# Performance work log

Hardware: AMD Instinct MI355X
Metric: run time of the kernel (lower is better)

## Reference

```python
import jax, jax.numpy as jnp
import numpy as np

N_NODES = 1000
N_EDGES = 8000
IN_FEATS = 64
HID = 128
RDIM = HID // 2  # UniversalReadout output dim
EPS = 1e-5


def _lrelu(v):
    return jax.nn.leaky_relu(v, 0.01)


def setup_inputs() -> dict:
    key = jax.random.key(0)
    ks = jax.random.split(key, 16)
    B = 128
    node_feats = jax.random.normal(ks[0], (B * N_NODES, IN_FEATS), jnp.float32)
    edge_weights = jax.random.uniform(ks[1], (B * N_EDGES,), jnp.float32)
    g_weights = jax.random.uniform(ks[2], (B * N_NODES,), jnp.float32)
    src = jax.random.randint(ks[3], (N_EDGES,), 0, N_NODES)
    dst = jax.random.randint(ks[4], (N_EDGES,), 0, N_NODES)
    # GraphConv weights (in, out), kaiming-ish scale
    W1 = jax.random.normal(ks[5], (IN_FEATS, HID), jnp.float32) / np.sqrt(IN_FEATS)
    W2 = jax.random.normal(ks[6], (HID, HID), jnp.float32) / np.sqrt(HID)
    W3 = jax.random.normal(ks[7], (HID, HID), jnp.float32) / np.sqrt(HID)
    suppl = jnp.ones((3, N_EDGES), jnp.float32)           # suppl_weights_conv1..3
    AR = jnp.ones((4, N_NODES), jnp.float32)              # AR1..AR4 weights
    gn_gamma = jnp.ones((3, HID), jnp.float32)
    gn_beta = jnp.zeros((3, HID), jnp.float32)
    gn_alpha = jnp.ones((3, HID), jnp.float32)            # GraphNorm mean-scale
    phi_W = jax.random.normal(ks[8], (3, HID, HID), jnp.float32) / np.sqrt(HID)
    phi_b = jnp.zeros((3, HID), jnp.float32)
    rho_W = jax.random.normal(ks[9], (3, HID, RDIM), jnp.float32) / np.sqrt(HID)
    rho_b = jnp.zeros((3, RDIM), jnp.float32)
    return dict(node_feats=node_feats, edge_weights=edge_weights, g_weights=g_weights,
                W1=W1, W2=W2, W3=W3, suppl=suppl, AR=AR,
                gn_gamma=gn_gamma, gn_beta=gn_beta, gn_alpha=gn_alpha,
                phi_W=phi_W, phi_b=phi_b, rho_W=rho_W, rho_b=rho_b,
                src=src, dst=dst)


def _forward(node_feats, edge_weights, g_weights, W1, W2, W3, suppl, AR,
             gn_gamma, gn_beta, gn_alpha, phi_W, phi_b, rho_W, rho_b, src, dst):
    B = node_feats.shape[0] // N_NODES
    x = node_feats.reshape(B, N_NODES, -1)        # (B, N, F)
    gw = g_weights.reshape(B, N_NODES)            # (B, N)
    ew = edge_weights.reshape(B, N_EDGES)         # (B, E)

    # structural degree normalization (norm='both'), shared topology
    deg_out = jnp.maximum(jnp.zeros((N_NODES,), x.dtype).at[src].add(1.0), 1.0)
    deg_in = jnp.maximum(jnp.zeros((N_NODES,), x.dtype).at[dst].add(1.0), 1.0)
    n_out = deg_out ** -0.5
    n_in = deg_in ** -0.5

    def gconv(h, W, ew_l):
        hs = h * n_out[None, :, None]
        msgs = hs[:, src, :] * ew_l[:, :, None]                       # (B, E, D)
        agg = jnp.zeros_like(hs).at[:, dst].add(msgs)                  # scatter-add
        return (agg * n_in[None, :, None]) @ W

    def gnorm(h, i):
        mean = h.mean(axis=1, keepdims=True)
        sub = h - gn_alpha[i] * mean
        var = (sub * sub).mean(axis=1, keepdims=True)
        return gn_gamma[i] * sub * jax.lax.rsqrt(var + EPS) + gn_beta[i]

    def uro(h, i):  # UniversalReadout (deep-sets): per-node MLP -> sum -> MLP
        z = _lrelu(h @ phi_W[i] + phi_b[i]).sum(axis=1)
        return _lrelu(z @ rho_W[i] + rho_b[i])

    def wmean(h, ar):  # dgl.mean_nodes with node weight: mean over nodes of w*x
        w = gw * ar[None, :]
        return (w[:, :, None] * h).mean(axis=1)

    pieces = [wmean(x, AR[0])]
    h = x
    Ws = (W1, W2, W3)
    for i in range(3):
        h = _lrelu(gnorm(gconv(h, Ws[i], ew * suppl[i][None, :]), i))
        pieces.append(uro(h, i))
        pieces.append(wmean(h, AR[i + 1]))
    return _lrelu(jnp.concatenate(pieces, axis=-1))


def reference(node_feats, edge_weights, g_weights, W1, W2, W3, suppl, AR,
              gn_gamma, gn_beta, gn_alpha, phi_W, phi_b, rho_W, rho_b, src, dst):
    return _forward(node_feats, edge_weights, g_weights, W1, W2, W3, suppl, AR,
                    gn_gamma, gn_beta, gn_alpha, phi_W, phi_b, rho_W, rho_b, src, dst)
```

## Files before the change

kernel.cpp:

```cpp
#include <hip/hip_runtime.h>
#include <cstddef>

#define NN 1000
#define NE 8000
#define FIN 64
#define DH 128
#define RD 64
#define FEPS 1e-5f

typedef short short8 __attribute__((ext_vector_type(8)));
typedef float f32x4 __attribute__((ext_vector_type(4)));

__device__ __forceinline__ float lrelu(float x){ return x > 0.f ? x : 0.01f*x; }

__device__ __forceinline__ unsigned short f2b(float x){
  union { float f; unsigned int u; } v; v.f = x;
  unsigned int r = (v.u + 0x7fffu + ((v.u >> 16) & 1u)) >> 16;
  return (unsigned short)r;
}
__device__ __forceinline__ float b2f(unsigned int lo16){
  union { unsigned int u; float f; } v; v.u = lo16 << 16; return v.f;
}
__device__ __forceinline__ unsigned int pack2(float a, float b){
  return (unsigned int)f2b(a) | ((unsigned int)f2b(b) << 16);
}


__global__ __launch_bounds__(1024) void k_topo(const int* __restrict__ src,
                       const int* __restrict__ dst,
                       float* nout, float* nin, int* rp,
                       int* csr_s, int* csr_e, int* csr_d){
  __shared__ int sdo[1024], sdi[1024], ssc[1024], sfill[1024];
  int t = threadIdx.x;
  sdo[t] = 0; sdi[t] = 0;
  __syncthreads();
  for (int e = t; e < NE; e += 1024){
    atomicAdd(&sdo[src[e]], 1);
    atomicAdd(&sdi[dst[e]], 1);
  }
  __syncthreads();
  int d = sdi[t];
  ssc[t] = d; __syncthreads();
  for (int off = 1; off < 1024; off <<= 1){
    int v = (t >= off) ? ssc[t-off] : 0;
    __syncthreads();
    ssc[t] += v;
    __syncthreads();
  }
  int myrp = ssc[t] - d;
  if (t < NN){
    rp[t] = myrp;
    nin[t]  = rsqrtf((float)max(sdi[t], 1));
    nout[t] = rsqrtf((float)max(sdo[t], 1));
  }
  if (t == NN-1) rp[NN] = ssc[t];
  sfill[t] = myrp;
  __syncthreads();
  for (int e = t; e < NE; e += 1024){
    int dn = dst[e];
    int pos = atomicAdd(&sfill[dn], 1);
    csr_s[pos] = src[e];
    csr_e[pos] = e;
    csr_d[pos] = dn;
  }
}


__global__ __launch_bounds__(256) void k_edge(const float* __restrict__ ew,
        const float* __restrict__ sup, const float* __restrict__ nout,
        const float* __restrict__ nin, const int* __restrict__ csr_s,
        const int* __restrict__ csr_e, const int* __restrict__ csr_d,
        int2* __restrict__ ecl, int B){
  int bid = blockIdx.x, t = threadIdx.x;
  int layer, b, q;
  if ((B & 7) == 0){
    int xcd = bid & 7, r = bid >> 3;
    int bsub = r/12, rem = r - bsub*12;
    layer = rem >> 2; q = rem & 3; b = bsub*8 + xcd;
  } else {
    layer = bid/(4*B);
    int rem = bid - layer*4*B;
    b = rem >> 2; q = rem & 3;
  }
  const float* ewb  = ew  + (size_t)b*NE;
  const float* supl = sup + (size_t)layer*NE;
  int2* o = ecl + ((size_t)layer*B + b)*NE;
  for (int k = q*2000 + t; k < q*2000 + 2000; k += 256){
    int e = csr_e[k]; int s = csr_s[k];
    float wv = ewb[e]*supl[e]*nout[s]*nin[csr_d[k]];
    int2 v; v.x = s; v.y = __float_as_int(wv);
    o[k] = v;
  }
}


__global__ __launch_bounds__(256) void k_misc(
        const float* __restrict__ W1, const float* __restrict__ W2,
        const float* __restrict__ W3, const float* __restrict__ phiW,
        unsigned short* __restrict__ wt,
        const float* __restrict__ x, const float* __restrict__ gw,
        const float* __restrict__ AR, float* __restrict__ out, int B){
  __shared__ float red[4][64];
  int bid = blockIdx.x, t = threadIdx.x;
  if (bid < 352){
    int i = bid*256 + t;
    if (i < 8192){
      int n = i >> 6, k = i & 63;
      wt[i] = f2b(W1[k*128 + n]);
    } else if (i < 24576){
      int j = i - 8192; int n = j >> 7, k = j & 127;
      wt[i] = f2b(W2[k*128 + n]);
    } else if (i < 40960){
      int j = i - 24576; int n = j >> 7, k = j & 127;
      wt[i] = f2b(W3[k*128 + n]);
    } else if (i < 90112){
      int j = i - 40960; int m = j >> 14; int jj = j & 16383;
      int n = jj >> 7, k = jj & 127;
      wt[i] = f2b(phiW[m*16384 + k*128 + n]);
    }
  } else {
    int wb = bid - 352;
    int b = wb >> 2, q = wb & 3;
    int r = t >> 6, l = t & 63;
    float acc = 0.f;
    int v0 = q*250;
    for (int v = v0 + r; v < v0 + 250; v += 4)
      acc += gw[(size_t)b*NN + v]*AR[v]*x[((size_t)b*NN + v)*FIN + l];
    red[r][l] = acc;
    __syncthreads();
    if (t < 64){
      float s = red[0][t]+red[1][t]+red[2][t]+red[3][t];
      atomicAdd(&out[(size_t)b*640 + t], s*(1.f/NN));
    }
  }
}


__global__ __launch_bounds__(256) void k_gath0(const float* __restrict__ x,
        const int2* __restrict__ ec, const int* __restrict__ rp,
        unsigned short* __restrict__ agg, int B){
  int bid = blockIdx.x;
  int b, chunk;
  if ((B & 7) == 0){
    int xcd = bid & 7, r = bid >> 3;
    int bsub = r/63; chunk = r - bsub*63; b = bsub*8 + xcd;
  } else { b = bid/63; chunk = bid - b*63; }
  int t = threadIdx.x;
  int grp = t >> 4, j = t & 15;
  int v = chunk*16 + grp; if (v >= NN) v = NN-1;
  int kb = rp[v], ke = rp[v+1];
  const float* xb = x + (size_t)b*NN*FIN;
  const int2* ecb = ec + (size_t)b*NE;
  float a0[4] = {0.f,0.f,0.f,0.f}, a1[4] = {0.f,0.f,0.f,0.f};
  int k = kb;
  for (; k+1 < ke; k += 2){
    int2 e0 = ecb[k], e1 = ecb[k+1];
    float4 x0 = *(const float4*)(xb + e0.x*FIN + j*4);
    float4 x1 = *(const float4*)(xb + e1.x*FIN + j*4);
    float w0 = __int_as_float(e0.y), w1 = __int_as_float(e1.y);
    a0[0] = fmaf(x0.x, w0, a0[0]); a0[1] = fmaf(x0.y, w0, a0[1]);
    a0[2] = fmaf(x0.z, w0, a0[2]); a0[3] = fmaf(x0.w, w0, a0[3]);
    a1[0] = fmaf(x1.x, w1, a1[0]); a1[1] = fmaf(x1.y, w1, a1[1]);
    a1[2] = fmaf(x1.z, w1, a1[2]); a1[3] = fmaf(x1.w, w1, a1[3]);
  }
  if (k < ke){
    int2 e0 = ecb[k];
    float4 x0 = *(const float4*)(xb + e0.x*FIN + j*4);
    float w0 = __int_as_float(e0.y);
    a0[0] = fmaf(x0.x, w0, a0[0]); a0[1] = fmaf(x0.y, w0, a0[1]);
    a0[2] = fmaf(x0.z, w0, a0[2]); a0[3] = fmaf(x0.w, w0, a0[3]);
  }
  uint2 o;
  o.x = pack2(a0[0]+a1[0], a0[1]+a1[1]);
  o.y = pack2(a0[2]+a1[2], a0[3]+a1[3]);
  *(uint2*)(agg + ((size_t)b*NN + v)*FIN + j*4) = o;
}


__global__ __launch_bounds__(256) void k_gathB(const unsigned short* __restrict__ h,
        const int2* __restrict__ ec, const int* __restrict__ rp,
        unsigned short* __restrict__ agg, int B){
  int bid = blockIdx.x;
  int b, chunk;
  if ((B & 7) == 0){
    int xcd = bid & 7, r = bid >> 3;
    int bsub = r/63; chunk = r - bsub*63; b = bsub*8 + xcd;
  } else { b = bid/63; chunk = bid - b*63; }
  int t = threadIdx.x;
  int grp = t >> 4, j = t & 15;
  int v = chunk*16 + grp; if (v >= NN) v = NN-1;
  int kb = rp[v], ke = rp[v+1];
  const unsigned short* hb = h + (size_t)b*NN*DH;
  const int2* ecb = ec + (size_t)b*NE;
  float a0[8] = {0.f,0.f,0.f,0.f,0.f,0.f,0.f,0.f};
  float a1[8] = {0.f,0.f,0.f,0.f,0.f,0.f,0.f,0.f};
  int k = kb;
  for (; k+1 < ke; k += 2){
    int2 e0 = ecb[k], e1 = ecb[k+1];
    uint4 u0 = *(const uint4*)(hb + e0.x*DH + j*8);
    uint4 u1 = *(const uint4*)(hb + e1.x*DH + j*8);
    float w0 = __int_as_float(e0.y), w1 = __int_as_float(e1.y);
    a0[0] = fmaf(b2f(u0.x & 0xffffu), w0, a0[0]);
    a0[1] = fmaf(b2f(u0.x >> 16),     w0, a0[1]);
    a0[2] = fmaf(b2f(u0.y & 0xffffu), w0, a0[2]);
    a0[3] = fmaf(b2f(u0.y >> 16),     w0, a0[3]);
    a0[4] = fmaf(b2f(u0.z & 0xffffu), w0, a0[4]);
    a0[5] = fmaf(b2f(u0.z >> 16),     w0, a0[5]);
    a0[6] = fmaf(b2f(u0.w & 0xffffu), w0, a0[6]);
    a0[7] = fmaf(b2f(u0.w >> 16),     w0, a0[7]);
    a1[0] = fmaf(b2f(u1.x & 0xffffu), w1, a1[0]);
    a1[1] = fmaf(b2f(u1.x >> 16),     w1, a1[1]);
    a1[2] = fmaf(b2f(u1.y & 0xffffu), w1, a1[2]);
    a1[3] = fmaf(b2f(u1.y >> 16),     w1, a1[3]);
    a1[4] = fmaf(b2f(u1.z & 0xffffu), w1, a1[4]);
    a1[5] = fmaf(b2f(u1.z >> 16),     w1, a1[5]);
    a1[6] = fmaf(b2f(u1.w & 0xffffu), w1, a1[6]);
    a1[7] = fmaf(b2f(u1.w >> 16),     w1, a1[7]);
  }
  if (k < ke){
    int2 e0 = ecb[k];
    uint4 u0 = *(const uint4*)(hb + e0.x*DH + j*8);
    float w0 = __int_as_float(e0.y);
    a0[0] = fmaf(b2f(u0.x & 0xffffu), w0, a0[0]);
    a0[1] = fmaf(b2f(u0.x >> 16),     w0, a0[1]);
    a0[2] = fmaf(b2f(u0.y & 0xffffu), w0, a0[2]);
    a0[3] = fmaf(b2f(u0.y >> 16),     w0, a0[3]);
    a0[4] = fmaf(b2f(u0.z & 0xffffu), w0, a0[4]);
    a0[5] = fmaf(b2f(u0.z >> 16),     w0, a0[5]);
    a0[6] = fmaf(b2f(u0.w & 0xffffu), w0, a0[6]);
    a0[7] = fmaf(b2f(u0.w >> 16),     w0, a0[7]);
  }
  uint4 o;
  o.x = pack2(a0[0]+a1[0], a0[1]+a1[1]);
  o.y = pack2(a0[2]+a1[2], a0[3]+a1[3]);
  o.z = pack2(a0[4]+a1[4], a0[5]+a1[5]);
  o.w = pack2(a0[6]+a1[6], a0[7]+a1[7]);
  *(uint4*)(agg + ((size_t)b*NN + v)*DH + j*8) = o;
}


template<int K>
__global__ __launch_bounds__(256) void k_conv(const unsigned short* __restrict__ A,
        const unsigned short* __restrict__ Wt, unsigned short* __restrict__ Cb,
        float* __restrict__ red_out, int B){
  constexpr int K2 = K*2;
  constexpr int CPR = K/8;
  __shared__ __align__(16) char smem[64*K2 + 128*K2];
  char* sA = smem;
  char* sW = smem + 64*K2;
  int t = threadIdx.x;
  int b, tile;
  if ((B & 7) == 0){
    int xcd = blockIdx.x & 7, r = blockIdx.x >> 3;
    int bsub = r >> 4; tile = r & 15; b = bsub*8 + xcd;
  } else { b = blockIdx.x >> 4; tile = blockIdx.x & 15; }
  int rows = NN - tile*64; if (rows > 64) rows = 64;
  size_t row0 = (size_t)b*NN + tile*64;
  size_t Mtot = (size_t)B*NN;

  for (int i = t; i < 64*CPR; i += 256){
    int r = i/CPR, cb = i%CPR;
    size_t gr = row0 + r; if (gr >= Mtot) gr = Mtot - 1;
    uint4 v = *(const uint4*)(A + gr*K + cb*8);
    *(uint4*)(sA + r*K2 + ((cb*16) ^ ((r & 7) << 4))) = v;
  }
  for (int i = t; i < 128*CPR; i += 256){
    int n = i/CPR, cb = i%CPR;
    uint4 v = *(const uint4*)(Wt + n*K + cb*8);
    *(uint4*)(sW + n*K2 + ((cb*16) ^ ((n & 7) << 4))) = v;
  }
  __syncthreads();

  int w = t >> 6, l = t & 63;
  int lr = l & 15, lk = l >> 4;
  f32x4 acc[8] = {};
  int arow = w*16 + lr;
  #pragma unroll
  for (int kk = 0; kk < K/32; ++kk){
    int kb = kk*64 + lk*16;
    short8 a = *(const short8*)(sA + arow*K2 + (kb ^ ((arow & 7) << 4)));
    #pragma unroll
    for (int f = 0; f < 8; ++f){
      int n = f*16 + lr;
      short8 bf = *(const short8*)(sW + n*K2 + (kb ^ ((n & 7) << 4)));
      acc[f] = __builtin_amdgcn_mfma_f32_16x16x32_bf16(a, bf, acc[f], 0, 0, 0);
    }
  }
  __syncthreads();

  float* red = (float*)smem;
  float cs[8], cq[8];
  int rbase = w*16 + lk*4;
  #pragma unroll
  for (int f = 0; f < 8; ++f){
    int col = f*16 + lr;
    float s = 0.f, q = 0.f;
    #pragma unroll
    for (int r = 0; r < 4; ++r){
      int row = rbase + r;
      bool ok = row < rows;
      float v = acc[f][r];
      if (ok) Cb[(row0 + row)*DH + col] = f2b(v);
      s += ok ? v : 0.f;
      q += ok ? v*v : 0.f;
    }
    s += __shfl_xor(s, 16); s += __shfl_xor(s, 32);
    q += __shfl_xor(q, 16); q += __shfl_xor(q, 32);
    cs[f] = s; cq[f] = q;
  }
  if (l < 16){
    #pragma unroll
    for (int f = 0; f < 8; ++f){
      red[w*128 + f*16 + l] = cs[f];
      red[512 + w*128 + f*16 + l] = cq[f];
    }
  }
  __syncthreads();
  if (t < 128){
    float s = red[t] + red[128+t] + red[256+t] + red[384+t];
    atomicAdd(&red_out[(size_t)b*DH + t], s);
    float q = red[512+t] + red[640+t] + red[768+t] + red[896+t];
    atomicAdd(&red_out[(size_t)B*DH + (size_t)b*DH + t], q);
  }
}


__global__ void k_finstats(const float* __restrict__ ssum, const float* __restrict__ ssq,
                           const float* __restrict__ alpha, const float* __restrict__ gamma,
                           const float* __restrict__ beta,
                           float* __restrict__ ivg, float* __restrict__ pc, int BD){
  int i = blockIdx.x*blockDim.x + threadIdx.x;
  if (i < BD){
    int d = i & (DH-1);
    float m   = ssum[i] * (1.f/NN);
    float ex2 = ssq [i] * (1.f/NN);
    float a = alpha[d];
    float var = ex2 - (2.f*a - a*a)*m*m;
    float g = gamma[d]*rsqrtf(var + FEPS);
    ivg[i] = g;
    pc [i] = beta[d] - a*m*g;
  }
}


__global__ __launch_bounds__(256) void k_phi(const unsigned short* __restrict__ hpre,
        const unsigned short* __restrict__ Wt, const float* __restrict__ ivg,
        const float* __restrict__ pc, const float* __restrict__ bias,
        const float* __restrict__ gw, const float* __restrict__ ar,
        unsigned short* __restrict__ hnorm,
        float* __restrict__ zout, float* __restrict__ out, int off, int B){
  __shared__ __align__(16) char smem[64*256 + 128*256];
  __shared__ float sgw[64];
  char* sA = smem;
  char* sW = smem + 64*256;
  int t = threadIdx.x;
  int b, tile;
  if ((B & 7) == 0){
    int xcd = blockIdx.x & 7, r = blockIdx.x >> 3;
    int bsub = r >> 4; tile = r & 15; b = bsub*8 + xcd;
  } else { b = blockIdx.x >> 4; tile = blockIdx.x & 15; }
  int rows = NN - tile*64; if (rows > 64) rows = 64;
  size_t row0 = (size_t)b*NN + tile*64;

  for (int i = t; i < 64*16; i += 256){
    int r = i >> 4, cb = i & 15;
    int rr = (r < rows) ? r : 0;
    uint4 u = *(const uint4*)(hpre + (row0 + rr)*DH + cb*8);
    int c0 = b*DH + cb*8;
    float4 g1 = *(const float4*)(ivg + c0), g2 = *(const float4*)(ivg + c0 + 4);
    float4 p1 = *(const float4*)(pc + c0),  p2 = *(const float4*)(pc + c0 + 4);
    float xv[8];
    xv[0] = b2f(u.x & 0xffffu); xv[1] = b2f(u.x >> 16);
    xv[2] = b2f(u.y & 0xffffu); xv[3] = b2f(u.y >> 16);
    xv[4] = b2f(u.z & 0xffffu); xv[5] = b2f(u.z >> 16);
    xv[6] = b2f(u.w & 0xffffu); xv[7] = b2f(u.w >> 16);
    float gg[8] = {g1.x,g1.y,g1.z,g1.w,g2.x,g2.y,g2.z,g2.w};
    float pv[8] = {p1.x,p1.y,p1.z,p1.w,p2.x,p2.y,p2.z,p2.w};
    float nv[8];
    #pragma unroll
    for (int d2 = 0; d2 < 8; ++d2){
      float n0 = fmaf(xv[d2], gg[d2], pv[d2]);
      nv[d2] = fmaxf(n0, 0.01f*n0);
    }
    uint4 o;
    o.x = pack2(nv[0],nv[1]); o.y = pack2(nv[2],nv[3]);
    o.z = pack2(nv[4],nv[5]); o.w = pack2(nv[6],nv[7]);
    *(uint4*)(sA + r*256 + ((cb*16) ^ ((r & 7) << 4))) = o;
    if (r < rows) *(uint4*)(hnorm + (row0 + r)*DH + cb*8) = o;
  }
  for (int i = t; i < 128*16; i += 256){
    int n = i >> 4, cb = i & 15;
    uint4 v = *(const uint4*)(Wt + n*DH + cb*8);
    *(uint4*)(sW + n*256 + ((cb*16) ^ ((n & 7) << 4))) = v;
  }
  if (t < 64){
    int vr = tile*64 + t;
    sgw[t] = (vr < NN) ? gw[(size_t)b*NN + vr]*ar[vr] : 0.f;
  }
  __syncthreads();

  int w = t >> 6, l = t & 63;
  int lr = l & 15, lk = l >> 4;
  f32x4 acc[8] = {};
  int arow = w*16 + lr;
  #pragma unroll
  for (int kk = 0; kk < 4; ++kk){
    int kb = kk*64 + lk*16;
    short8 a = *(const short8*)(sA + arow*256 + (kb ^ ((arow & 7) << 4)));
    #pragma unroll
    for (int f = 0; f < 8; ++f){
      int n = f*16 + lr;
      short8 bf = *(const short8*)(sW + n*256 + (kb ^ ((n & 7) << 4)));
      acc[f] = __builtin_amdgcn_mfma_f32_16x16x32_bf16(a, bf, acc[f], 0, 0, 0);
    }
  }
  __syncthreads();

  float* red = (float*)sW;
  float cs[8];
  int rbase = w*16 + lk*4;
  #pragma unroll
  for (int f = 0; f < 8; ++f){
    int col = f*16 + lr;
    float bv = bias[col];
    float s = 0.f;
    #pragma unroll
    for (int r = 0; r < 4; ++r){
      int row = rbase + r;
      float u = lrelu(acc[f][r] + bv);
      s += (row < rows) ? u : 0.f;
    }
    s += __shfl_xor(s, 16); s += __shfl_xor(s, 32);
    cs[f] = s;
  }
  if (l < 16){
    #pragma unroll
    for (int f = 0; f < 8; ++f) red[w*128 + f*16 + l] = cs[f];
  }
  __syncthreads();
  if (t < 128){
    float s = red[t] + red[128+t] + red[256+t] + red[384+t];
    atomicAdd(&zout[(size_t)b*DH + t], s);
  } else {
    int col = t - 128;
    float s = 0.f;
    for (int r = 0; r < 64; ++r){
      int byteoff = r*256 + (((col >> 3)*16) ^ ((r & 7) << 4)) + (col & 7)*2;
      s += sgw[r]*b2f(*(const unsigned short*)(sA + byteoff));
    }
    atomicAdd(&out[(size_t)b*640 + off + col], s*(1.f/NN));
  }
}


__global__ void k_rho(const float* __restrict__ statz, const float* __restrict__ rhoW,
                      const float* __restrict__ rhob, float* __restrict__ out, int B){
  int i = blockIdx.x / B, b = blockIdx.x % B;
  int d = threadIdx.x;
  const float* z = statz + (size_t)i*3*B*DH + (size_t)2*B*DH + (size_t)b*DH;
  float acc = rhob[i*RD + d];
  const float* Wm = rhoW + (size_t)i*DH*RD;
  for (int k = 0; k < DH; ++k) acc = fmaf(z[k], Wm[k*RD + d], acc);
  out[(size_t)b*640 + 64 + i*192 + d] = lrelu(acc);
}

__global__ void k_flrelu(float* o, int n){
  int i = blockIdx.x*blockDim.x + threadIdx.x;
  if (i < n) o[i] = lrelu(o[i]);
}


extern "C" void kernel_launch(void* const* d_in, const int* in_sizes, int n_in,
                              void* d_out, int out_size, void* d_ws, size_t ws_size,
                              hipStream_t stream){
  const float* x    = (const float*)d_in[0];
  const float* ew   = (const float*)d_in[1];
  const float* gw   = (const float*)d_in[2];
  const float* W1   = (const float*)d_in[3];
  const float* W2   = (const float*)d_in[4];
  const float* W3   = (const float*)d_in[5];
  const float* sup  = (const float*)d_in[6];
  const float* AR   = (const float*)d_in[7];
  const float* gam  = (const float*)d_in[8];
  const float* bet  = (const float*)d_in[9];
  const float* alp  = (const float*)d_in[10];
  const float* phiW = (const float*)d_in[11];
  const float* phib = (const float*)d_in[12];
  const float* rhoW = (const float*)d_in[13];
  const float* rhob = (const float*)d_in[14];
  const int*   src  = (const int*)d_in[15];
  const int*   dst  = (const int*)d_in[16];
  float* out = (float*)d_out;

  int B = in_sizes[0] / (NN*FIN);
  size_t M = (size_t)B*NN;
  size_t BD = (size_t)B*DH;

  float* w = (float*)d_ws;
  size_t p = 0;
  float* nout = w+p; p += 1024;
  float* nin  = w+p; p += 1024;
  int* rp     = (int*)(w+p); p += 1024;
  int* csr_s  = (int*)(w+p); p += 8192;
  int* csr_e  = (int*)(w+p); p += 8192;
  int* csr_d  = (int*)(w+p); p += 8192;
  float* statz = w+p; p += 3*3*BD;
  float* ivgP = w+p; p += 3*BD;
  float* pP   = w+p; p += 3*BD;
  unsigned short* wt = (unsigned short*)(w+p); p += 45056;
  int2* ecl   = (int2*)(w+p); p += (size_t)6*B*NE;
  unsigned short* hpre  = (unsigned short*)(w+p); p += M*DH/2;
  unsigned short* hnorm = (unsigned short*)(w+p); p += M*DH/2;
  unsigned short* agg   = (unsigned short*)(w+p); p += M*DH/2;

  hipMemsetAsync(out, 0, (size_t)out_size*sizeof(float), stream);
  hipMemsetAsync(statz, 0, 9*BD*sizeof(float), stream);

  k_topo<<<1, 1024, 0, stream>>>(src, dst, nout, nin, rp, csr_s, csr_e, csr_d);
  k_edge<<<12*B, 256, 0, stream>>>(ew, sup, nout, nin, csr_s, csr_e, csr_d, ecl, B);
  k_misc<<<352 + B*4, 256, 0, stream>>>(W1, W2, W3, phiW, wt, x, gw, AR, out, B);

  const int wt_off[3] = {0, 8192, 24576};

  for (int i = 0; i < 3; ++i){
    float* SS = statz + (size_t)i*3*BD;
    if (i == 0){
      k_gath0<<<B*63, 256, 0, stream>>>(x, ecl, rp, agg, B);
      k_conv<FIN><<<B*16, 256, 0, stream>>>(agg, wt, hpre, SS, B);
    } else {
      k_gathB<<<B*63, 256, 0, stream>>>(hnorm, ecl + (size_t)i*B*NE, rp, agg, B);
      k_conv<DH><<<B*16, 256, 0, stream>>>(agg, wt + wt_off[i], hpre, SS, B);
    }
    k_finstats<<<(int)((BD+255)/256), 256, 0, stream>>>(SS, SS + BD,
        alp + i*DH, gam + i*DH, bet + i*DH, ivgP + (size_t)i*BD, pP + (size_t)i*BD, (int)BD);
    k_phi<<<B*16, 256, 0, stream>>>(hpre, wt + 40960 + i*16384,
        ivgP + (size_t)i*BD, pP + (size_t)i*BD, phib + i*DH, gw, AR + (size_t)(i+1)*NN,
        hnorm, SS + 2*BD, out, 128 + i*192, B);
  }

  k_rho<<<3*B, RD, 0, stream>>>(statz, rhoW, rhob, out, B);
  k_flrelu<<<(B*640+255)/256, 256, 0, stream>>>(out, B*640);
}
```

Baseline: 309.5 us.

## Fuse GraphNorm stat finalization into phi, gather layer-0 from bf16 features

Drops the separate k_finstats launch and computes the per-graph scale and shift directly into shared memory inside k_phi. The k_misc weighted-mean pass now also writes a bf16 copy of the input features, so the layer-0 gather reads half the bytes per edge. Both gather kernels are unrolled to four independent edges with separate accumulators for more memory-level parallelism, and k_misc gets an XCD-aware block mapping. The costs are an extra bf16 write of x, earlier rounding of layer-0 inputs, and redundant stat computation in each phi block.

Measured after the change: 308.5 us. No clear change (-0.3%).

```diff
diff --git a/kernel.cpp b/kernel.cpp
--- a/kernel.cpp
+++ b/kernel.cpp
@@ -98,8 +98,9 @@
         const float* __restrict__ W1, const float* __restrict__ W2,
         const float* __restrict__ W3, const float* __restrict__ phiW,
         unsigned short* __restrict__ wt,
-        const float* __restrict__ x, const float* __restrict__ gw,
-        const float* __restrict__ AR, float* __restrict__ out, int B){
+        const float* __restrict__ x, unsigned short* __restrict__ xbf,
+        const float* __restrict__ gw, const float* __restrict__ AR,
+        float* __restrict__ out, int B){
   __shared__ float red[4][64];
   int bid = blockIdx.x, t = threadIdx.x;
   if (bid < 352){
@@ -120,12 +121,20 @@
     }
   } else {
     int wb = bid - 352;
-    int b = wb >> 2, q = wb & 3;
+    int b, q;
+    if ((B & 7) == 0){
+      int xcd = wb & 7, r = wb >> 3;
+      int bsub = r >> 2; q = r & 3; b = bsub*8 + xcd;
+    } else { b = wb >> 2; q = wb & 3; }
     int r = t >> 6, l = t & 63;
     float acc = 0.f;
     int v0 = q*250;
-    for (int v = v0 + r; v < v0 + 250; v += 4)
-      acc += gw[(size_t)b*NN + v]*AR[v]*x[((size_t)b*NN + v)*FIN + l];
+    for (int v = v0 + r; v < v0 + 250; v += 4){
+      size_t idx = ((size_t)b*NN + v)*FIN + l;
+      float xv = x[idx];
+      xbf[idx] = f2b(xv);
+      acc += gw[(size_t)b*NN + v]*AR[v]*xv;
+    }
     red[r][l] = acc;
     __syncthreads();
     if (t < 64){
@@ -136,7 +145,7 @@
 }
 
 
-__global__ __launch_bounds__(256) void k_gath0(const float* __restrict__ x,
+__global__ __launch_bounds__(256) void k_gathF(const unsigned short* __restrict__ xbf,
         const int2* __restrict__ ec, const int* __restrict__ rp,
         unsigned short* __restrict__ agg, int B){
   int bid = blockIdx.x;
@@ -149,30 +158,36 @@
   int grp = t >> 4, j = t & 15;
   int v = chunk*16 + grp; if (v >= NN) v = NN-1;
   int kb = rp[v], ke = rp[v+1];
-  const float* xb = x + (size_t)b*NN*FIN;
+  const unsigned short* xb = xbf + (size_t)b*NN*FIN;
   const int2* ecb = ec + (size_t)b*NE;
-  float a0[4] = {0.f,0.f,0.f,0.f}, a1[4] = {0.f,0.f,0.f,0.f};
+  float acc[4][4] = {};
   int k = kb;
-  for (; k+1 < ke; k += 2){
-    int2 e0 = ecb[k], e1 = ecb[k+1];
-    float4 x0 = *(const float4*)(xb + e0.x*FIN + j*4);
-    float4 x1 = *(const float4*)(xb + e1.x*FIN + j*4);
-    float w0 = __int_as_float(e0.y), w1 = __int_as_float(e1.y);
-    a0[0] = fmaf(x0.x, w0, a0[0]); a0[1] = fmaf(x0.y, w0, a0[1]);
-    a0[2] = fmaf(x0.z, w0, a0[2]); a0[3] = fmaf(x0.w, w0, a0[3]);
-    a1[0] = fmaf(x1.x, w1, a1[0]); a1[1] = fmaf(x1.y, w1, a1[1]);
-    a1[2] = fmaf(x1.z, w1, a1[2]); a1[3] = fmaf(x1.w, w1, a1[3]);
-  }
-  if (k < ke){
-    int2 e0 = ecb[k];
-    float4 x0 = *(const float4*)(xb + e0.x*FIN + j*4);
-    float w0 = __int_as_float(e0.y);
-    a0[0] = fmaf(x0.x, w0, a0[0]); a0[1] = fmaf(x0.y, w0, a0[1]);
-    a0[2] = fmaf(x0.z, w0, a0[2]); a0[3] = fmaf(x0.w, w0, a0[3]);
+  for (; k+3 < ke; k += 4){
+    #pragma unroll
+    for (int uu = 0; uu < 4; ++uu){
+      int2 e = ecb[k+uu];
+      uint2 u = *(const uint2*)(xb + e.x*FIN + j*4);
+      float wgt = __int_as_float(e.y);
+      acc[uu][0] = fmaf(b2f(u.x & 0xffffu), wgt, acc[uu][0]);
+      acc[uu][1] = fmaf(b2f(u.x >> 16),     wgt, acc[uu][1]);
+      acc[uu][2] = fmaf(b2f(u.y & 0xffffu), wgt, acc[uu][2]);
+      acc[uu][3] = fmaf(b2f(u.y >> 16),     wgt, acc[uu][3]);
+    }
+  }
+  for (; k < ke; ++k){
+    int2 e = ecb[k];
+    uint2 u = *(const uint2*)(xb + e.x*FIN + j*4);
+    float wgt = __int_as_float(e.y);
+    acc[0][0] = fmaf(b2f(u.x & 0xffffu), wgt, acc[0][0]);
+    acc[0][1] = fmaf(b2f(u.x >> 16),     wgt, acc[0][1]);
+    acc[0][2] = fmaf(b2f(u.y & 0xffffu), wgt, acc[0][2]);
+    acc[0][3] = fmaf(b2f(u.y >> 16),     wgt, acc[0][3]);
   }
   uint2 o;
-  o.x = pack2(a0[0]+a1[0], a0[1]+a1[1]);
-  o.y = pack2(a0[2]+a1[2], a0[3]+a1[3]);
+  o.x = pack2(acc[0][0]+acc[1][0]+acc[2][0]+acc[3][0],
+              acc[0][1]+acc[1][1]+acc[2][1]+acc[3][1]);
+  o.y = pack2(acc[0][2]+acc[1][2]+acc[2][2]+acc[3][2],
+              acc[0][3]+acc[1][3]+acc[2][3]+acc[3][3]);
   *(uint2*)(agg + ((size_t)b*NN + v)*FIN + j*4) = o;
 }
 
@@ -192,49 +207,44 @@
   int kb = rp[v], ke = rp[v+1];
   const unsigned short* hb = h + (size_t)b*NN*DH;
   const int2* ecb = ec + (size_t)b*NE;
-  float a0[8] = {0.f,0.f,0.f,0.f,0.f,0.f,0.f,0.f};
-  float a1[8] = {0.f,0.f,0.f,0.f,0.f,0.f,0.f,0.f};
+  float acc[4][8] = {};
   int k = kb;
-  for (; k+1 < ke; k += 2){
-    int2 e0 = ecb[k], e1 = ecb[k+1];
-    uint4 u0 = *(const uint4*)(hb + e0.x*DH + j*8);
-    uint4 u1 = *(const uint4*)(hb + e1.x*DH + j*8);
-    float w0 = __int_as_float(e0.y), w1 = __int_as_float(e1.y);
-    a0[0] = fmaf(b2f(u0.x & 0xffffu), w0, a0[0]);
-    a0[1] = fmaf(b2f(u0.x >> 16),     w0, a0[1]);
-    a0[2] = fmaf(b2f(u0.y & 0xffffu), w0, a0[2]);
-    a0[3] = fmaf(b2f(u0.y >> 16),     w0, a0[3]);
-    a0[4] = fmaf(b2f(u0.z & 0xffffu), w0, a0[4]);
-    a0[5] = fmaf(b2f(u0.z >> 16),     w0, a0[5]);
-    a0[6] = fmaf(b2f(u0.w & 0xffffu), w0, a0[6]);
-    a0[7] = fmaf(b2f(u0.w >> 16),     w0, a0[7]);
-    a1[0] = fmaf(b2f(u1.x & 0xffffu), w1, a1[0]);
-    a1[1] = fmaf(b2f(u1.x >> 16),     w1, a1[1]);
-    a1[2] = fmaf(b2f(u1.y & 0xffffu), w1, a1[2]);
-    a1[3] = fmaf(b2f(u1.y >> 16),     w1, a1[3]);
-    a1[4] = fmaf(b2f(u1.z & 0xffffu), w1, a1[4]);
-    a1[5] = fmaf(b2f(u1.z >> 16),     w1, a1[5]);
-    a1[6] = fmaf(b2f(u1.w & 0xffffu), w1, a1[6]);
-    a1[7] = fmaf(b2f(u1.w >> 16),     w1, a1[7]);
-  }
-  if (k < ke){
-    int2 e0 = ecb[k];
-    uint4 u0 = *(const uint4*)(hb + e0.x*DH + j*8);
-    float w0 = __int_as_float(e0.y);
-    a0[0] = fmaf(b2f(u0.x & 0xffffu), w0, a0[0]);
-    a0[1] = fmaf(b2f(u0.x >> 16),     w0, a0[1]);
-    a0[2] = fmaf(b2f(u0.y & 0xffffu), w0, a0[2]);
-    a0[3] = fmaf(b2f(u0.y >> 16),     w0, a0[3]);
-    a0[4] = fmaf(b2f(u0.z & 0xffffu), w0, a0[4]);
-    a0[5] = fmaf(b2f(u0.z >> 16),     w0, a0[5]);
-    a0[6] = fmaf(b2f(u0.w & 0xffffu), w0, a0[6]);
-    a0[7] = fmaf(b2f(u0.w >> 16),     w0, a0[7]);
-  }
+  for (; k+3 < ke; k += 4){
+    #pragma unroll
+    for (int uu = 0; uu < 4; ++uu){
+      int2 e = ecb[k+uu];
+      uint4 u = *(const uint4*)(hb + e.x*DH + j*8);
+      float wgt = __int_as_float(e.y);
+      acc[uu][0] = fmaf(b2f(u.x & 0xffffu), wgt, acc[uu][0]);
+      acc[uu][1] = fmaf(b2f(u.x >> 16),     wgt, acc[uu][1]);
+      acc[uu][2] = fmaf(b2f(u.y & 0xffffu), wgt, acc[uu][2]);
+      acc[uu][3] = fmaf(b2f(u.y >> 16),     wgt, acc[uu][3]);
+      acc[uu][4] = fmaf(b2f(u.z & 0xffffu), wgt, acc[uu][4]);
+      acc[uu][5] = fmaf(b2f(u.z >> 16),     wgt, acc[uu][5]);
+      acc[uu][6] = fmaf(b2f(u.w & 0xffffu), wgt, acc[uu][6]);
+      acc[uu][7] = fmaf(b2f(u.w >> 16),     wgt, acc[uu][7]);
+    }
+  }
+  for (; k < ke; ++k){
+    int2 e = ecb[k];
+    uint4 u = *(const uint4*)(hb + e.x*DH + j*8);
+    float wgt = __int_as_float(e.y);
+    acc[0][0] = fmaf(b2f(u.x & 0xffffu), wgt, acc[0][0]);
+    acc[0][1] = fmaf(b2f(u.x >> 16),     wgt, acc[0][1]);
+    acc[0][2] = fmaf(b2f(u.y & 0xffffu), wgt, acc[0][2]);
+    acc[0][3] = fmaf(b2f(u.y >> 16),     wgt, acc[0][3]);
+    acc[0][4] = fmaf(b2f(u.z & 0xffffu), wgt, acc[0][4]);
+    acc[0][5] = fmaf(b2f(u.z >> 16),     wgt, acc[0][5]);
+    acc[0][6] = fmaf(b2f(u.w & 0xffffu), wgt, acc[0][6]);
+    acc[0][7] = fmaf(b2f(u.w >> 16),     wgt, acc[0][7]);
+  }
+  float f[8];
+  #pragma unroll
+  for (int d2 = 0; d2 < 8; ++d2)
+    f[d2] = acc[0][d2]+acc[1][d2]+acc[2][d2]+acc[3][d2];
   uint4 o;
-  o.x = pack2(a0[0]+a1[0], a0[1]+a1[1]);
-  o.y = pack2(a0[2]+a1[2], a0[3]+a1[3]);
-  o.z = pack2(a0[4]+a1[4], a0[5]+a1[5]);
-  o.w = pack2(a0[6]+a1[6], a0[7]+a1[7]);
+  o.x = pack2(f[0],f[1]); o.y = pack2(f[2],f[3]);
+  o.z = pack2(f[4],f[5]); o.w = pack2(f[6],f[7]);
   *(uint4*)(agg + ((size_t)b*NN + v)*DH + j*8) = o;
 }
 
@@ -325,31 +335,16 @@
 }
 
 
-__global__ void k_finstats(const float* __restrict__ ssum, const float* __restrict__ ssq,
-                           const float* __restrict__ alpha, const float* __restrict__ gamma,
-                           const float* __restrict__ beta,
-                           float* __restrict__ ivg, float* __restrict__ pc, int BD){
-  int i = blockIdx.x*blockDim.x + threadIdx.x;
-  if (i < BD){
-    int d = i & (DH-1);
-    float m   = ssum[i] * (1.f/NN);
-    float ex2 = ssq [i] * (1.f/NN);
-    float a = alpha[d];
-    float var = ex2 - (2.f*a - a*a)*m*m;
-    float g = gamma[d]*rsqrtf(var + FEPS);
-    ivg[i] = g;
-    pc [i] = beta[d] - a*m*g;
-  }
-}
-
-
 __global__ __launch_bounds__(256) void k_phi(const unsigned short* __restrict__ hpre,
-        const unsigned short* __restrict__ Wt, const float* __restrict__ ivg,
-        const float* __restrict__ pc, const float* __restrict__ bias,
+        const unsigned short* __restrict__ Wt,
+        const float* __restrict__ ssum, const float* __restrict__ ssq,
+        const float* __restrict__ alpha, const float* __restrict__ gamma,
+        const float* __restrict__ beta, const float* __restrict__ bias,
         const float* __restrict__ gw, const float* __restrict__ ar,
         unsigned short* __restrict__ hnorm,
         float* __restrict__ zout, float* __restrict__ out, int off, int B){
   __shared__ __align__(16) char smem[64*256 + 128*256];
+  __shared__ __align__(16) float sivg[128], spc[128];
   __shared__ float sgw[64];
   char* sA = smem;
   char* sW = smem + 64*256;
@@ -362,13 +357,27 @@
   int rows = NN - tile*64; if (rows > 64) rows = 64;
   size_t row0 = (size_t)b*NN + tile*64;
 
+  if (t < 128){
+    float m   = ssum[(size_t)b*DH + t]*(1.f/NN);
+    float ex2 = ssq [(size_t)b*DH + t]*(1.f/NN);
+    float a = alpha[t];
+    float var = ex2 - (2.f*a - a*a)*m*m;
+    float g = gamma[t]*rsqrtf(var + FEPS);
+    sivg[t] = g;
+    spc [t] = beta[t] - a*m*g;
+  } else if (t < 192){
+    int vr = tile*64 + (t - 128);
+    sgw[t-128] = (vr < NN) ? gw[(size_t)b*NN + vr]*ar[vr] : 0.f;
+  }
+  __syncthreads();
+
   for (int i = t; i < 64*16; i += 256){
     int r = i >> 4, cb = i & 15;
     int rr = (r < rows) ? r : 0;
     uint4 u = *(const uint4*)(hpre + (row0 + rr)*DH + cb*8);
-    int c0 = b*DH + cb*8;
-    float4 g1 = *(const float4*)(ivg + c0), g2 = *(const float4*)(ivg + c0 + 4);
-    float4 p1 = *(const float4*)(pc + c0),  p2 = *(const float4*)(pc + c0 + 4);
+    int c0 = cb*8;
+    float4 g1 = *(const float4*)(sivg + c0), g2 = *(const float4*)(sivg + c0 + 4);
+    float4 p1 = *(const float4*)(spc + c0),  p2 = *(const float4*)(spc + c0 + 4);
     float xv[8];
     xv[0] = b2f(u.x & 0xffffu); xv[1] = b2f(u.x >> 16);
     xv[2] = b2f(u.y & 0xffffu); xv[3] = b2f(u.y >> 16);
@@ -392,10 +401,6 @@
     int n = i >> 4, cb = i & 15;
     uint4 v = *(const uint4*)(Wt + n*DH + cb*8);
     *(uint4*)(sW + n*256 + ((cb*16) ^ ((n & 7) << 4))) = v;
-  }
-  if (t < 64){
-    int vr = tile*64 + t;
-    sgw[t] = (vr < NN) ? gw[(size_t)b*NN + vr]*ar[vr] : 0.f;
   }
   __syncthreads();
 
@@ -505,10 +510,9 @@
   int* csr_e  = (int*)(w+p); p += 8192;
   int* csr_d  = (int*)(w+p); p += 8192;
   float* statz = w+p; p += 3*3*BD;
-  float* ivgP = w+p; p += 3*BD;
-  float* pP   = w+p; p += 3*BD;
   unsigned short* wt = (unsigned short*)(w+p); p += 45056;
   int2* ecl   = (int2*)(w+p); p += (size_t)6*B*NE;
+  unsigned short* xbf   = (unsigned short*)(w+p); p += M*FIN/2;
   unsigned short* hpre  = (unsigned short*)(w+p); p += M*DH/2;
   unsigned short* hnorm = (unsigned short*)(w+p); p += M*DH/2;
   unsigned short* agg   = (unsigned short*)(w+p); p += M*DH/2;
@@ -518,24 +522,22 @@
 
   k_topo<<<1, 1024, 0, stream>>>(src, dst, nout, nin, rp, csr_s, csr_e, csr_d);
   k_edge<<<12*B, 256, 0, stream>>>(ew, sup, nout, nin, csr_s, csr_e, csr_d, ecl, B);
-  k_misc<<<352 + B*4, 256, 0, stream>>>(W1, W2, W3, phiW, wt, x, gw, AR, out, B);
+  k_misc<<<352 + B*4, 256, 0, stream>>>(W1, W2, W3, phiW, wt, x, xbf, gw, AR, out, B);
 
   const int wt_off[3] = {0, 8192, 24576};
 
   for (int i = 0; i < 3; ++i){
     float* SS = statz + (size_t)i*3*BD;
     if (i == 0){
-      k_gath0<<<B*63, 256, 0, stream>>>(x, ecl, rp, agg, B);
+      k_gathF<<<B*63, 256, 0, stream>>>(xbf, ecl, rp, agg, B);
       k_conv<FIN><<<B*16, 256, 0, stream>>>(agg, wt, hpre, SS, B);
     } else {
       k_gathB<<<B*63, 256, 0, stream>>>(hnorm, ecl + (size_t)i*B*NE, rp, agg, B);
       k_conv<DH><<<B*16, 256, 0, stream>>>(agg, wt + wt_off[i], hpre, SS, B);
     }
-    k_finstats<<<(int)((BD+255)/256), 256, 0, stream>>>(SS, SS + BD,
-        alp + i*DH, gam + i*DH, bet + i*DH, ivgP + (size_t)i*BD, pP + (size_t)i*BD, (int)BD);
     k_phi<<<B*16, 256, 0, stream>>>(hpre, wt + 40960 + i*16384,
-        ivgP + (size_t)i*BD, pP + (size_t)i*BD, phib + i*DH, gw, AR + (size_t)(i+1)*NN,
-        hnorm, SS + 2*BD, out, 128 + i*192, B);
+        SS, SS + BD, alp + i*DH, gam + i*DH, bet + i*DH, phib + i*DH,
+        gw, AR + (size_t)(i+1)*NN, hnorm, SS + 2*BD, out, 128 + i*192, B);
   }
 
   k_rho<<<3*B, RD, 0, stream>>>(statz, rhoW, rhob, out, B);
```
